# Performance work log

Hardware: AMD Instinct MI355X
Metric: run time of the kernel (lower is better)

The kernel has to match this reference:

```python
import math
import jax, jax.numpy as jnp
import numpy as np

B, S, HID = 4, 2048, 1024
H, D = 16, 64  # num_head, head_dim
EPS = 1e-12  # F.normalize eps


def _qknorm(t, gamma):
    # t: [B, S, H, D]; F.normalize(dim=-1) * sqrt(D) * gamma[None]
    norm = jnp.sqrt(jnp.sum(t * t, axis=-1, keepdims=True))
    t = t / jnp.maximum(norm, EPS)
    return t * math.sqrt(D) * gamma  # gamma broadcasts over [B,S]


def setup_inputs() -> dict:
    key = jax.random.key(0)
    ks = jax.random.split(key, 8)
    s = 0.02
    return {
        "x": jax.random.normal(ks[0], (B, S, HID), jnp.float32),
        "q_w": jax.random.normal(ks[1], (HID, HID), jnp.float32) * s,
        "q_b": jnp.zeros((HID,), jnp.float32),
        "kv_w": jax.random.normal(ks[2], (2 * HID, HID), jnp.float32) * s,
        "kv_b": jnp.zeros((2 * HID,), jnp.float32),
        "gamma_q": jnp.ones((H, D), jnp.float32),
        "gamma_k": jnp.ones((H, D), jnp.float32),
        "out_w": jax.random.normal(ks[3], (HID, HID), jnp.float32) * s,
    }


def reference(x, q_w, q_b, kv_w, kv_b, gamma_q, gamma_k, out_w):
    # self-attention: context = x
    q = (x @ q_w.T + q_b).reshape(B, S, H, D)
    kv = x @ kv_w.T + kv_b  # [B, S, 2*HID]
    k, v = jnp.split(kv, 2, axis=-1)
    k = k.reshape(B, S, H, D)
    v = v.reshape(B, S, H, D)
    q = _qknorm(q, gamma_q)
    k = _qknorm(k, gamma_k)
    scores = jnp.einsum('bqhd,bkhd->bhqk', q, k)  # [B,H,S,S]
    attn = jax.nn.softmax(scores, axis=-1)
    out = jnp.einsum('bhqk,bkhd->bqhd', attn, v).reshape(B, S, HID)
    return out @ out_w.T
```

## Files before the change

kernel.cpp:

```cpp
#include <hip/hip_runtime.h>
#include <stdint.h>

#define B_ 4
#define S_ 2048
#define HID_ 1024
#define NH_ 16
#define HD_ 64

typedef __bf16 bf16x8 __attribute__((ext_vector_type(8)));
typedef __bf16 bf16x4 __attribute__((ext_vector_type(4)));
typedef float f32x4 __attribute__((ext_vector_type(4)));

__device__ inline void gload_lds16(const void* g, void* l) {
  __builtin_amdgcn_global_load_lds((const __attribute__((address_space(1))) unsigned int*)g,
                                   (__attribute__((address_space(3))) unsigned int*)l, 16, 0, 0);
}

__device__ inline f32x4 fmax4(f32x4 a, f32x4 b) {
  f32x4 r;
  r[0] = fmaxf(a[0], b[0]); r[1] = fmaxf(a[1], b[1]);
  r[2] = fmaxf(a[2], b[2]); r[3] = fmaxf(a[3], b[3]);
  return r;
}

__global__ __launch_bounds__(256) void cvt_bf16(const float* __restrict__ in, __bf16* __restrict__ out) {
  int i = (blockIdx.x * 256 + threadIdx.x) * 4;
  f32x4 v = *(const f32x4*)(in + i);
  bf16x4 o;
  o[0] = (__bf16)v[0]; o[1] = (__bf16)v[1]; o[2] = (__bf16)v[2]; o[3] = (__bf16)v[3];
  *(bf16x4*)(out + i) = o;
}

template <int MODE>
__global__ __launch_bounds__(256) void gemm_bt(const __bf16* __restrict__ A,
                                               const __bf16* __restrict__ Bt,
                                               const float* __restrict__ bias_q,
                                               const float* __restrict__ bias_kv,
                                               const float* __restrict__ gamma_q,
                                               const float* __restrict__ gamma_k,
                                               __bf16* __restrict__ Cq,
                                               __bf16* __restrict__ Ck,
                                               float* __restrict__ Cf,
                                               __bf16* __restrict__ vt,
                                               int M, int N, int K, int gx) {
  const int nwg = gridDim.x;
  const int lin = blockIdx.x;
  const int swz = (lin & 7) * (nwg >> 3) + (lin >> 3);
  const int n0 = (swz % gx) * 128;
  const int m0 = (swz / gx) * 128;
  const int tid  = threadIdx.x;
  const int wave = tid >> 6, lane = tid & 63;
  const int wm = wave >> 1, wn = wave & 1;
  const int lrow = lane & 15, lgrp = lane >> 4;

  __shared__ __bf16 sA[128][64];
  __shared__ __bf16 sB[128][64];

  f32x4 acc[4][4];
#pragma unroll
  for (int i = 0; i < 4; i++)
#pragma unroll
    for (int j = 0; j < 4; j++) acc[i][j] = f32x4{0.f, 0.f, 0.f, 0.f};

  for (int k0 = 0; k0 < K; k0 += 64) {
    __syncthreads();
#pragma unroll
    for (int c = 0; c < 4; c++) {
      const int row = wave * 32 + c * 8;
      const __bf16* ga = A + (size_t)(m0 + row + (lane >> 3)) * K + k0 + (lane & 7) * 8;
      gload_lds16(ga, &sA[row][0]);
      const __bf16* gb = Bt + (size_t)(n0 + row + (lane >> 3)) * K + k0 + (lane & 7) * 8;
      gload_lds16(gb, &sB[row][0]);
    }
    __syncthreads();
#pragma unroll
    for (int kk = 0; kk < 2; kk++) {
      bf16x8 af[4], bfr[4];
#pragma unroll
      for (int i = 0; i < 4; i++) {
        af[i]  = *(const bf16x8*)(&sA[wm * 64 + i * 16 + lrow][kk * 32 + 8 * lgrp]);
        bfr[i] = *(const bf16x8*)(&sB[wn * 64 + i * 16 + lrow][kk * 32 + 8 * lgrp]);
      }
#pragma unroll
      for (int i = 0; i < 4; i++)
#pragma unroll
        for (int j = 0; j < 4; j++)
          acc[i][j] = __builtin_amdgcn_mfma_f32_16x16x32_bf16(af[i], bfr[j], acc[i][j], 0, 0, 0);
    }
  }

  if (MODE == 4) {
    float bv[4];
#pragma unroll
    for (int j = 0; j < 4; j++) {
      const int n = n0 + wn * 64 + j * 16 + lrow;
      bv[j] = (n < 1024) ? bias_q[n] : bias_kv[n - 1024];
    }
#pragma unroll
    for (int i = 0; i < 4; i++)
#pragma unroll
      for (int j = 0; j < 4; j++)
#pragma unroll
        for (int r = 0; r < 4; r++) acc[i][j][r] += bv[j];

    const int nblk = n0 >> 10;
    if (nblk < 2) {
      const float nscale = (nblk == 0) ? 8.f * 1.44269504f : 8.f;
      const float* gam = (nblk == 0) ? gamma_q : gamma_k;
      __bf16* dst = (nblk == 0) ? Cq : Ck;
      float g[4];
#pragma unroll
      for (int j = 0; j < 4; j++) g[j] = gam[(n0 + wn * 64 + j * 16 + lrow) & 1023];
#pragma unroll
      for (int i = 0; i < 4; i++) {
#pragma unroll
        for (int r = 0; r < 4; r++) {
          float ss = acc[i][0][r] * acc[i][0][r] + acc[i][1][r] * acc[i][1][r] +
                     acc[i][2][r] * acc[i][2][r] + acc[i][3][r] * acc[i][3][r];
#pragma unroll
          for (int off = 1; off < 16; off <<= 1) ss += __shfl_xor(ss, off, 64);
          const float inv = nscale / fmaxf(sqrtf(ss), 1e-12f);
          const int m = m0 + wm * 64 + i * 16 + lgrp * 4 + r;
#pragma unroll
          for (int j = 0; j < 4; j++) {
            const int n = (n0 + wn * 64 + j * 16 + lrow) & 1023;
            dst[(size_t)m * 1024 + n] = (__bf16)(acc[i][j][r] * inv * g[j]);
          }
        }
      }
    } else {
#pragma unroll
      for (int i = 0; i < 4; i++) {
#pragma unroll
        for (int j = 0; j < 4; j++) {
          const int nn = n0 + wn * 64 + j * 16 + lrow - 2048;
          const int h = nn >> 6, d = nn & 63;
          const int m = m0 + wm * 64 + i * 16 + lgrp * 4;
          const int b = m >> 11, s0 = m & 2047;
          bf16x4 pk;
#pragma unroll
          for (int r = 0; r < 4; r++) pk[r] = (__bf16)acc[i][j][r];
          *(bf16x4*)(vt + ((size_t)((b * 16 + h) * 64 + d)) * 2048 + s0) = pk;
        }
      }
    }
  } else {
#pragma unroll
    for (int i = 0; i < 4; i++)
#pragma unroll
      for (int j = 0; j < 4; j++) {
        const int n = n0 + wn * 64 + j * 16 + lrow;
#pragma unroll
        for (int r = 0; r < 4; r++) {
          const int m = m0 + wm * 64 + i * 16 + lgrp * 4 + r;
          Cf[(size_t)m * N + n] = acc[i][j][r];
        }
      }
  }
}

__global__ __launch_bounds__(512) void attn_kernel(const __bf16* __restrict__ qm,
                                                   const __bf16* __restrict__ km,
                                                   const __bf16* __restrict__ vtm,
                                                   __bf16* __restrict__ o) {
  constexpr float THR = 11.5416f;
  const int lin = blockIdx.y * gridDim.x + blockIdx.x;
  const int swz = (lin & 7) * 128 + (lin >> 3);
  const int qb = swz & 15;
  const int bh = swz >> 4;
  const int b = bh >> 4, h = bh & 15;
  const int q0 = qb * 128;
  const int tid = threadIdx.x, wave = tid >> 6, lane = tid & 63;
  const int lrow = lane & 15, lgrp = lane >> 4;

  __shared__ __bf16 sK[2][64 * 64];
  __shared__ __bf16 sVt[2][64 * 64];
  __shared__ __bf16 sP[8][16 * 64];

  const __bf16* kbase  = km + (size_t)(b * S_) * 1024 + h * 64;
  const __bf16* vtbase = vtm + (size_t)((b * 16 + h) * 64) * 2048;

  const int srow = lane >> 3;
  const int pchunk = lane & 7;

  auto stage = [&](int buf, int kt) {
    const int rr = wave * 8;
    const int r = rr + srow;
    gload_lds16(kbase + (size_t)(kt * 64 + r) * 1024 + ((pchunk ^ (r & 7)) << 3),
                &sK[buf][rr * 64]);
    gload_lds16(vtbase + (size_t)r * 2048 + kt * 64 + ((pchunk ^ (r & 7)) << 3),
                &sVt[buf][rr * 64]);
  };

  bf16x8 qf[2];
  {
    const __bf16* qp = qm + (size_t)(b * S_ + q0 + wave * 16 + lrow) * 1024 + h * 64;
    qf[0] = *(const bf16x8*)(qp + 8 * lgrp);
    qf[1] = *(const bf16x8*)(qp + 32 + 8 * lgrp);
  }

  f32x4 accd[4];
#pragma unroll
  for (int dt = 0; dt < 4; ++dt) accd[dt] = f32x4{0.f, 0.f, 0.f, 0.f};
  float m_r = -1e30f, l_r = 0.f;

  stage(0, 0);
  int buf = 0;
  for (int kt = 0; kt < S_ / 64; ++kt) {
    __syncthreads();
    if (kt + 1 < S_ / 64) stage(buf ^ 1, kt + 1);

    f32x4 sc[4];
#pragma unroll
    for (int t = 0; t < 4; ++t) sc[t] = f32x4{0.f, 0.f, 0.f, 0.f};
    __builtin_amdgcn_s_setprio(1);
#pragma unroll
    for (int t = 0; t < 4; ++t) {
      const int krow = t * 16 + lrow;
#pragma unroll
      for (int kk = 0; kk < 2; ++kk) {
        bf16x8 kf = *(const bf16x8*)(&sK[buf][krow * 64 + (((kk * 4 + lgrp) ^ (krow & 7)) << 3)]);
        sc[t] = __builtin_amdgcn_mfma_f32_16x16x32_bf16(kf, qf[kk], sc[t], 0, 0, 0);
      }
    }
    __builtin_amdgcn_s_setprio(0);

    f32x4 mm = fmax4(fmax4(sc[0], sc[1]), fmax4(sc[2], sc[3]));
    float tm = fmaxf(fmaxf(mm[0], mm[1]), fmaxf(mm[2], mm[3]));
    tm = fmaxf(tm, __shfl_xor(tm, 16, 64));
    tm = fmaxf(tm, __shfl_xor(tm, 32, 64));

    if (!__all(tm - m_r <= THR)) {
      const float mn = fmaxf(m_r, tm);
      const float scl = __builtin_exp2f(m_r - mn);
      m_r = mn;
      l_r *= scl;
      float sclr[4];
#pragma unroll
      for (int j = 0; j < 4; ++j) sclr[j] = __shfl(scl, lgrp * 4 + j, 64);
#pragma unroll
      for (int dt = 0; dt < 4; ++dt)
#pragma unroll
        for (int j = 0; j < 4; ++j) accd[dt][j] *= sclr[j];
    }

    const float nm = m_r;
    float ps0 = 0.f, ps1 = 0.f;
#pragma unroll
    for (int t = 0; t < 4; ++t) {
      bf16x4 pk;
      const float p0 = __builtin_exp2f(sc[t][0] - nm);
      const float p1 = __builtin_exp2f(sc[t][1] - nm);
      const float p2 = __builtin_exp2f(sc[t][2] - nm);
      const float p3 = __builtin_exp2f(sc[t][3] - nm);
      ps0 += p0 + p2; ps1 += p1 + p3;
      pk[0] = (__bf16)p0; pk[1] = (__bf16)p1; pk[2] = (__bf16)p2; pk[3] = (__bf16)p3;
      *(bf16x4*)(&sP[wave][lrow * 64 + (((2 * t + (lgrp >> 1)) ^ (lrow & 7)) << 3) +
                           ((lgrp & 1) << 2)]) = pk;
    }
    float ps = ps0 + ps1;
    ps += __shfl_xor(ps, 16, 64);
    ps += __shfl_xor(ps, 32, 64);
    l_r += ps;

    __builtin_amdgcn_s_setprio(1);
#pragma unroll
    for (int half = 0; half < 2; ++half) {
      bf16x8 pf = *(const bf16x8*)(&sP[wave][lrow * 64 + (((half * 4 + lgrp) ^ (lrow & 7)) << 3)]);
#pragma unroll
      for (int dt = 0; dt < 4; ++dt) {
        const int d = dt * 16 + lrow;
        bf16x8 vf = *(const bf16x8*)(&sVt[buf][d * 64 + (((half * 4 + lgrp) ^ (d & 7)) << 3)]);
        accd[dt] = __builtin_amdgcn_mfma_f32_16x16x32_bf16(pf, vf, accd[dt], 0, 0, 0);
      }
    }
    __builtin_amdgcn_s_setprio(0);
    buf ^= 1;
  }

#pragma unroll
  for (int j = 0; j < 4; ++j) {
    const float lv = __shfl(l_r, lgrp * 4 + j, 64);
    const float inv = 1.f / lv;
    const int row = b * S_ + q0 + wave * 16 + lgrp * 4 + j;
    __bf16* ob = o + (size_t)row * 1024 + h * 64;
#pragma unroll
    for (int dt = 0; dt < 4; ++dt) ob[dt * 16 + lrow] = (__bf16)(accd[dt][j] * inv);
  }
}

extern "C" void kernel_launch(void* const* d_in, const int* in_sizes, int n_in,
                              void* d_out, int out_size, void* d_ws, size_t ws_size,
                              hipStream_t stream) {
  (void)in_sizes; (void)n_in; (void)out_size; (void)ws_size;
  const float* x       = (const float*)d_in[0];
  const float* q_w     = (const float*)d_in[1];
  const float* q_b     = (const float*)d_in[2];
  const float* kv_w    = (const float*)d_in[3];
  const float* kv_b    = (const float*)d_in[4];
  const float* gamma_q = (const float*)d_in[5];
  const float* gamma_k = (const float*)d_in[6];
  const float* out_w   = (const float*)d_in[7];
  float* out = (float*)d_out;

  char* ws = (char*)d_ws;
  __bf16* x_bf   = (__bf16*)(ws);
  __bf16* qkvw_bf = (__bf16*)(ws + (16ull << 20));
  __bf16* ow_bf  = (__bf16*)(ws + (22ull << 20));
  __bf16* q_bf   = (__bf16*)(ws + (24ull << 20));
  __bf16* k_bf   = (__bf16*)(ws + (40ull << 20));
  __bf16* vt_bf  = (__bf16*)(ws + (56ull << 20));
  __bf16* at_bf  = (__bf16*)(ws + (72ull << 20));

  cvt_bf16<<<8192, 256, 0, stream>>>(x, x_bf);
  cvt_bf16<<<1024, 256, 0, stream>>>(q_w, qkvw_bf);
  cvt_bf16<<<2048, 256, 0, stream>>>(kv_w, qkvw_bf + (1024ull * 1024));
  cvt_bf16<<<1024, 256, 0, stream>>>(out_w, ow_bf);

  gemm_bt<4><<<1536, 256, 0, stream>>>(x_bf, qkvw_bf, q_b, kv_b, gamma_q, gamma_k,
                                       q_bf, k_bf, nullptr, vt_bf, 8192, 3072, 1024, 24);

  attn_kernel<<<dim3(16, 64), 512, 0, stream>>>(q_bf, k_bf, vt_bf, at_bf);

  gemm_bt<1><<<512, 256, 0, stream>>>(at_bf, ow_bf, nullptr, nullptr, nullptr, nullptr,
                                      nullptr, nullptr, out, nullptr, 8192, 1024, 1024, 8);
}
```

Baseline: 348.2 us.

## Double attention query tile to 256 rows and compute row sums via MFMA

The attention kernel now runs 1024-thread blocks covering 256 query rows per (batch, head). Each K/V tile staged into shared memory is therefore reused by twice as many waves. Staging is split so half the waves load K and half load V^T. The softmax row sum is no longer a scalar reduction with cross-lane shuffles; an extra MFMA against a vector of ones accumulates it alongside the PV product. The risk is fewer blocks in the grid, larger LDS use per block and higher register pressure under the 1024-thread launch bound, and the sum now comes from the bf16-rounded probabilities.

```diff
diff --git a/kernel.cpp b/kernel.cpp
--- a/kernel.cpp
+++ b/kernel.cpp
@@ -159,23 +159,23 @@
   }
 }
 
-__global__ __launch_bounds__(512) void attn_kernel(const __bf16* __restrict__ qm,
-                                                   const __bf16* __restrict__ km,
-                                                   const __bf16* __restrict__ vtm,
-                                                   __bf16* __restrict__ o) {
+__global__ __launch_bounds__(1024) void attn_kernel(const __bf16* __restrict__ qm,
+                                                    const __bf16* __restrict__ km,
+                                                    const __bf16* __restrict__ vtm,
+                                                    __bf16* __restrict__ o) {
   constexpr float THR = 11.5416f;
   const int lin = blockIdx.y * gridDim.x + blockIdx.x;
-  const int swz = (lin & 7) * 128 + (lin >> 3);
-  const int qb = swz & 15;
-  const int bh = swz >> 4;
+  const int swz = (lin & 7) * 64 + (lin >> 3);
+  const int qb = swz & 7;
+  const int bh = swz >> 3;
   const int b = bh >> 4, h = bh & 15;
-  const int q0 = qb * 128;
+  const int q0 = qb * 256;
   const int tid = threadIdx.x, wave = tid >> 6, lane = tid & 63;
   const int lrow = lane & 15, lgrp = lane >> 4;
 
   __shared__ __bf16 sK[2][64 * 64];
   __shared__ __bf16 sVt[2][64 * 64];
-  __shared__ __bf16 sP[8][16 * 64];
+  __shared__ __bf16 sP[16][16 * 64];
 
   const __bf16* kbase  = km + (size_t)(b * S_) * 1024 + h * 64;
   const __bf16* vtbase = vtm + (size_t)((b * 16 + h) * 64) * 2048;
@@ -184,12 +184,15 @@
   const int pchunk = lane & 7;
 
   auto stage = [&](int buf, int kt) {
-    const int rr = wave * 8;
+    const int rr = (wave & 7) * 8;
     const int r = rr + srow;
-    gload_lds16(kbase + (size_t)(kt * 64 + r) * 1024 + ((pchunk ^ (r & 7)) << 3),
-                &sK[buf][rr * 64]);
-    gload_lds16(vtbase + (size_t)r * 2048 + kt * 64 + ((pchunk ^ (r & 7)) << 3),
-                &sVt[buf][rr * 64]);
+    if (wave < 8) {
+      gload_lds16(kbase + (size_t)(kt * 64 + r) * 1024 + ((pchunk ^ (r & 7)) << 3),
+                  &sK[buf][rr * 64]);
+    } else {
+      gload_lds16(vtbase + (size_t)r * 2048 + kt * 64 + ((pchunk ^ (r & 7)) << 3),
+                  &sVt[buf][rr * 64]);
+    }
   };
 
   bf16x8 qf[2];
@@ -199,10 +202,15 @@
     qf[1] = *(const bf16x8*)(qp + 32 + 8 * lgrp);
   }
 
-  f32x4 accd[4];
+  bf16x8 ones;
+#pragma unroll
+  for (int i = 0; i < 8; i++) ones[i] = (__bf16)1.f;
+
+  f32x4 accd[4], accl;
 #pragma unroll
   for (int dt = 0; dt < 4; ++dt) accd[dt] = f32x4{0.f, 0.f, 0.f, 0.f};
-  float m_r = -1e30f, l_r = 0.f;
+  accl = f32x4{0.f, 0.f, 0.f, 0.f};
+  float m_r = -1e30f;
 
   stage(0, 0);
   int buf = 0;
@@ -234,7 +242,6 @@
       const float mn = fmaxf(m_r, tm);
       const float scl = __builtin_exp2f(m_r - mn);
       m_r = mn;
-      l_r *= scl;
       float sclr[4];
 #pragma unroll
       for (int j = 0; j < 4; ++j) sclr[j] = __shfl(scl, lgrp * 4 + j, 64);
@@ -242,31 +249,27 @@
       for (int dt = 0; dt < 4; ++dt)
 #pragma unroll
         for (int j = 0; j < 4; ++j) accd[dt][j] *= sclr[j];
+#pragma unroll
+      for (int j = 0; j < 4; ++j) accl[j] *= sclr[j];
     }
 
     const float nm = m_r;
-    float ps0 = 0.f, ps1 = 0.f;
 #pragma unroll
     for (int t = 0; t < 4; ++t) {
       bf16x4 pk;
-      const float p0 = __builtin_exp2f(sc[t][0] - nm);
-      const float p1 = __builtin_exp2f(sc[t][1] - nm);
-      const float p2 = __builtin_exp2f(sc[t][2] - nm);
-      const float p3 = __builtin_exp2f(sc[t][3] - nm);
-      ps0 += p0 + p2; ps1 += p1 + p3;
-      pk[0] = (__bf16)p0; pk[1] = (__bf16)p1; pk[2] = (__bf16)p2; pk[3] = (__bf16)p3;
+      pk[0] = (__bf16)__builtin_exp2f(sc[t][0] - nm);
+      pk[1] = (__bf16)__builtin_exp2f(sc[t][1] - nm);
+      pk[2] = (__bf16)__builtin_exp2f(sc[t][2] - nm);
+      pk[3] = (__bf16)__builtin_exp2f(sc[t][3] - nm);
       *(bf16x4*)(&sP[wave][lrow * 64 + (((2 * t + (lgrp >> 1)) ^ (lrow & 7)) << 3) +
                            ((lgrp & 1) << 2)]) = pk;
     }
-    float ps = ps0 + ps1;
-    ps += __shfl_xor(ps, 16, 64);
-    ps += __shfl_xor(ps, 32, 64);
-    l_r += ps;
 
     __builtin_amdgcn_s_setprio(1);
 #pragma unroll
     for (int half = 0; half < 2; ++half) {
       bf16x8 pf = *(const bf16x8*)(&sP[wave][lrow * 64 + (((half * 4 + lgrp) ^ (lrow & 7)) << 3)]);
+      accl = __builtin_amdgcn_mfma_f32_16x16x32_bf16(pf, ones, accl, 0, 0, 0);
 #pragma unroll
       for (int dt = 0; dt < 4; ++dt) {
         const int d = dt * 16 + lrow;
@@ -280,8 +283,7 @@
 
 #pragma unroll
   for (int j = 0; j < 4; ++j) {
-    const float lv = __shfl(l_r, lgrp * 4 + j, 64);
-    const float inv = 1.f / lv;
+    const float inv = 1.f / accl[j];
     const int row = b * S_ + q0 + wave * 16 + lgrp * 4 + j;
     __bf16* ob = o + (size_t)row * 1024 + h * 64;
 #pragma unroll
@@ -320,7 +322,7 @@
   gemm_bt<4><<<1536, 256, 0, stream>>>(x_bf, qkvw_bf, q_b, kv_b, gamma_q, gamma_k,
                                        q_bf, k_bf, nullptr, vt_bf, 8192, 3072, 1024, 24);
 
-  attn_kernel<<<dim3(16, 64), 512, 0, stream>>>(q_bf, k_bf, vt_bf, at_bf);
+  attn_kernel<<<dim3(8, 64), 1024, 0, stream>>>(q_bf, k_bf, vt_bf, at_bf);
 
   gemm_bt<1><<<512, 256, 0, stream>>>(at_bf, ow_bf, nullptr, nullptr, nullptr, nullptr,
                                       nullptr, nullptr, out, nullptr, 8192, 1024, 1024, 8);
```

Measured after the change: 343.4 us. No clear change (-1.4%).
